# Optimization experiments

Measured on AMD Instinct MI355X. Metric: run time of the kernel, lower is better.

## Reference

```python
import jax, jax.numpy as jnp
import numpy as np

B, S, IN, H, C, L = 128, 512, 128, 512, 1000, 2


def setup_inputs() -> dict:
    key = jax.random.key(0)
    ks = jax.random.split(key, 11)
    s_in = 1.0 / np.sqrt(H)
    inp = {"x": jax.random.normal(ks[0], (B, S, IN), dtype=jnp.float32)}
    # layer 0
    inp["W_ih0"] = jax.random.uniform(ks[1], (H, IN), minval=-s_in, maxval=s_in)
    inp["W_hh0"] = jax.random.uniform(ks[2], (H, H), minval=-s_in, maxval=s_in)
    inp["b_ih0"] = jax.random.uniform(ks[3], (H,), minval=-s_in, maxval=s_in)
    inp["b_hh0"] = jax.random.uniform(ks[4], (H,), minval=-s_in, maxval=s_in)
    # layer 1
    inp["W_ih1"] = jax.random.uniform(ks[5], (H, H), minval=-s_in, maxval=s_in)
    inp["W_hh1"] = jax.random.uniform(ks[6], (H, H), minval=-s_in, maxval=s_in)
    inp["b_ih1"] = jax.random.uniform(ks[7], (H,), minval=-s_in, maxval=s_in)
    inp["b_hh1"] = jax.random.uniform(ks[8], (H,), minval=-s_in, maxval=s_in)
    # output linear
    inp["W_out"] = jax.random.uniform(ks[9], (C, H), minval=-s_in, maxval=s_in)
    inp["b_out"] = jax.random.uniform(ks[10], (C,), minval=-s_in, maxval=s_in)
    return inp


def _rnn_layer(seq, W_ih, W_hh, b_ih, b_hh):
    # seq: [B, S, D_in] -> [B, S, H]; h_t = tanh(x_t W_ih^T + b_ih + h_{t-1} W_hh^T + b_hh)
    # precompute input projection for all timesteps (one big GEMM)
    xp = jnp.einsum('bsd,hd->bsh', seq, W_ih) + b_ih + b_hh  # [B, S, H]
    h0 = jnp.zeros((seq.shape[0], W_hh.shape[0]), dtype=seq.dtype)

    def step(h, xp_t):
        h_new = jnp.tanh(xp_t + h @ W_hh.T)
        return h_new, h_new

    _, hs = jax.lax.scan(step, h0, jnp.swapaxes(xp, 0, 1))  # hs: [S, B, H]
    return jnp.swapaxes(hs, 0, 1)


def reference(x, W_ih0, W_hh0, b_ih0, b_hh0, W_ih1, W_hh1, b_ih1, b_hh1, W_out, b_out):
    h = _rnn_layer(x, W_ih0, W_hh0, b_ih0, b_hh0)
    h = _rnn_layer(h, W_ih1, W_hh1, b_ih1, b_hh1)
    logits = h[:, -1, :] @ W_out.T + b_out  # [B, C]
    return jax.nn.log_softmax(logits, axis=-1)
```

## Files before the change

### kernel.cpp

```cpp
#include <hip/hip_runtime.h>


using short8  = __attribute__((ext_vector_type(8))) short;
using floatx4 = __attribute__((ext_vector_type(4))) float;
using i32x4   = __attribute__((ext_vector_type(4))) int;
using f32x4   = __attribute__((ext_vector_type(4))) float;

#define DEV static __device__ __forceinline__
#define PINA(x) asm volatile("" : "+a"(x))
#define PINV(x) asm volatile("" : "+v"(x))

#define TWO_LOG2E 2.8853900817779268f

DEV void lds_barrier() {
    asm volatile("s_waitcnt lgkmcnt(0)\n\ts_barrier" ::: "memory");
}

DEV unsigned short f2bf(float f) {
    union { float f; unsigned u; } v; v.f = f;
    unsigned r = (v.u + 0x7fffu + ((v.u >> 16) & 1u)) >> 16;
    return (unsigned short)r;
}

__global__ __launch_bounds__(64) void packi8_kernel(
    const float* __restrict__ W, signed char* __restrict__ Wq,
    float* __restrict__ sc2)
{
    const int j = blockIdx.x;
    const int t = threadIdx.x;
    const float* row = W + (size_t)j * 512;

    float4 a = *(const float4*)(row + t * 8);
    float4 b = *(const float4*)(row + t * 8 + 4);
    float m = fmaxf(fmaxf(fabsf(a.x), fabsf(a.y)), fmaxf(fabsf(a.z), fabsf(a.w)));
    m = fmaxf(m, fmaxf(fmaxf(fabsf(b.x), fabsf(b.y)), fmaxf(fabsf(b.z), fabsf(b.w))));
    #pragma unroll
    for (int off = 32; off; off >>= 1) m = fmaxf(m, __shfl_down(m, off, 64));
    m = __shfl(m, 0, 64);
    if (t == 0) sc2[j] = m * (1.0f / (127.f * 127.f)) * TWO_LOG2E;

    if (t < 32) {
        const int kt = t >> 2, lq = t & 3;
        const int jtg = j >> 4, lm = j & 15;
        const float r = 127.f / m;
        int w4[4];
        #pragma unroll
        for (int w = 0; w < 4; ++w) {
            int v = 0;
            #pragma unroll
            for (int e = 0; e < 4; ++e) {
                int q = __float2int_rn(row[kt * 64 + lq * 16 + w * 4 + e] * r);
                v |= (q & 255) << (8 * e);
            }
            w4[w] = v;
        }
        i32x4 pk; pk[0] = w4[0]; pk[1] = w4[1]; pk[2] = w4[2]; pk[3] = w4[3];
        *(i32x4*)(Wq + ((size_t)((jtg * 8 + kt) * 64 + lq * 16 + lm)) * 16) = pk;
    }
}

template <int K, int MODE>
__global__ __launch_bounds__(256, 2) void proj_kernel(
    const void* __restrict__ Aptr, const float* __restrict__ W,
    const float* __restrict__ b1, const float* __restrict__ b2,
    unsigned short* __restrict__ out, float oscale)
{
    constexpr int LDA = 40;
    __shared__ unsigned short As[128 * LDA];
    __shared__ unsigned short Ws[64 * LDA];

    const int tid  = threadIdx.x;
    const int lane = tid & 63, wave = tid >> 6;
    const int lm   = lane & 15, lq = lane >> 4;
    const int nbase = blockIdx.x * 64;
    const int mtile = blockIdx.y;
    const int mbase = mtile * 128;

    floatx4 acc[2][4] = {};

    const int ar = tid >> 1, ak = (tid & 1) * 16;
    const int wr = tid >> 2, wk = (tid & 3) * 8;

    for (int k0 = 0; k0 < K; k0 += 32) {
        if (MODE == 0) {
            const float* x   = (const float*)Aptr;
            const float* src = x + ((size_t)ar * 512 + mtile) * 128 + (k0 + ak);
            float4 f0 = *(const float4*)(src + 0);
            float4 f1 = *(const float4*)(src + 4);
            float4 f2 = *(const float4*)(src + 8);
            float4 f3 = *(const float4*)(src + 12);
            unsigned short* d = As + ar * LDA + ak;
            d[0]=f2bf(f0.x); d[1]=f2bf(f0.y); d[2]=f2bf(f0.z); d[3]=f2bf(f0.w);
            d[4]=f2bf(f1.x); d[5]=f2bf(f1.y); d[6]=f2bf(f1.z); d[7]=f2bf(f1.w);
            d[8]=f2bf(f2.x); d[9]=f2bf(f2.y); d[10]=f2bf(f2.z); d[11]=f2bf(f2.w);
            d[12]=f2bf(f3.x); d[13]=f2bf(f3.y); d[14]=f2bf(f3.z); d[15]=f2bf(f3.w);
        } else {
            const unsigned short* h =
                (const unsigned short*)Aptr + (size_t)(mbase + ar) * K + k0 + ak;
            short8 v0 = *(const short8*)(h);
            short8 v1 = *(const short8*)(h + 8);
            *(short8*)(As + ar * LDA + ak)     = v0;
            *(short8*)(As + ar * LDA + ak + 8) = v1;
        }
        {
            const float* src = W + (size_t)(nbase + wr) * K + k0 + wk;
            float4 f0 = *(const float4*)(src);
            float4 f1 = *(const float4*)(src + 4);
            unsigned short* d = Ws + wr * LDA + wk;
            d[0]=f2bf(f0.x); d[1]=f2bf(f0.y); d[2]=f2bf(f0.z); d[3]=f2bf(f0.w);
            d[4]=f2bf(f1.x); d[5]=f2bf(f1.y); d[6]=f2bf(f1.z); d[7]=f2bf(f1.w);
        }
        __syncthreads();

        short8 af0 = *(const short8*)(As + (wave * 32 +  0 + lm) * LDA + lq * 8);
        short8 af1 = *(const short8*)(As + (wave * 32 + 16 + lm) * LDA + lq * 8);
        #pragma unroll
        for (int nt = 0; nt < 4; ++nt) {
            short8 bf = *(const short8*)(Ws + (nt * 16 + lm) * LDA + lq * 8);
            acc[0][nt] = __builtin_amdgcn_mfma_f32_16x16x32_bf16(af0, bf, acc[0][nt], 0, 0, 0);
            acc[1][nt] = __builtin_amdgcn_mfma_f32_16x16x32_bf16(af1, bf, acc[1][nt], 0, 0, 0);
        }
        __syncthreads();
    }

    #pragma unroll
    for (int nt = 0; nt < 4; ++nt) {
        const int n = nbase + nt * 16 + lm;
        const float bias = b1[n] + b2[n];
        #pragma unroll
        for (int mt = 0; mt < 2; ++mt) {
            const int mrow = mbase + wave * 32 + mt * 16 + lq * 4;
            #pragma unroll
            for (int r = 0; r < 4; ++r)
                out[(size_t)(mrow + r) * 512 + n] = f2bf((acc[mt][nt][r] + bias) * oscale);
        }
    }
}


#define MFMA_J(JJ, BFR)                                                        \
  {                                                                            \
    acc[JJ] = __builtin_amdgcn_mfma_i32_16x16x64_i8(wa[JJ][0], BFR[0], z4, 0, 0, 0); \
    _Pragma("unroll")                                                          \
    for (int kt = 1; kt < 8; ++kt)                                             \
      acc[JJ] = __builtin_amdgcn_mfma_i32_16x16x64_i8(wa[JJ][kt], BFR[kt], acc[JJ], 0, 0, 0); \
  }

#define EPI_J(JJ, XVROW, HWBUF, TCUR)                                          \
  {                                                                            \
    const int jtg = wave * 4 + (JJ);                                           \
    float x0 = __uint_as_float(__builtin_amdgcn_perm(XVROW[JJ].x, 0u, 0x05040c0cu)); \
    float x1 = __uint_as_float(__builtin_amdgcn_perm(XVROW[JJ].x, 0u, 0x07060c0cu)); \
    float x2 = __uint_as_float(__builtin_amdgcn_perm(XVROW[JJ].y, 0u, 0x05040c0cu)); \
    float x3 = __uint_as_float(__builtin_amdgcn_perm(XVROW[JJ].y, 0u, 0x07060c0cu)); \
    float e0 = __builtin_amdgcn_exp2f(fmaf((float)acc[JJ][0], sc[JJ][0], x0));  \
    float e1 = __builtin_amdgcn_exp2f(fmaf((float)acc[JJ][1], sc[JJ][1], x1));  \
    float e2 = __builtin_amdgcn_exp2f(fmaf((float)acc[JJ][2], sc[JJ][2], x2));  \
    float e3 = __builtin_amdgcn_exp2f(fmaf((float)acc[JJ][3], sc[JJ][3], x3));  \
    float q0 = fmaf(-2.f, __builtin_amdgcn_rcpf(e0 + 1.f), 1.f);                \
    float q1 = fmaf(-2.f, __builtin_amdgcn_rcpf(e1 + 1.f), 1.f);                \
    float q2 = fmaf(-2.f, __builtin_amdgcn_rcpf(e2 + 1.f), 1.f);                \
    float q3 = fmaf(-2.f, __builtin_amdgcn_rcpf(e3 + 1.f), 1.f);                \
    unsigned m0 = __float_as_uint(fmaf(q0, 127.f, 12582912.f));                 \
    unsigned m1 = __float_as_uint(fmaf(q1, 127.f, 12582912.f));                 \
    unsigned m2 = __float_as_uint(fmaf(q2, 127.f, 12582912.f));                 \
    unsigned m3 = __float_as_uint(fmaf(q3, 127.f, 12582912.f));                 \
    unsigned lo = __builtin_amdgcn_perm(m1, m0, 0x00000400u);                   \
    unsigned hi = __builtin_amdgcn_perm(m3, m2, 0x00000400u);                   \
    unsigned qb = __builtin_amdgcn_perm(hi, lo, 0x05040100u);                   \
    *(unsigned*)((HWBUF) + lm * 512 + ((jtg ^ lm) << 4) + lq * 4) = qb;         \
    if (MODE == 0) {                                                            \
      if (lm < 2) {                                                             \
        uint2 st;                                                               \
        st.x = __builtin_amdgcn_perm(__float_as_uint(q1), __float_as_uint(q0), 0x07060302u); \
        st.y = __builtin_amdgcn_perm(__float_as_uint(q3), __float_as_uint(q2), 0x07060302u); \
        *(uint2*)(hst + (JJ) * 16) = st;                                        \
      }                                                                         \
    } else if ((TCUR) == 511) {                                                 \
      if (lm < 2) {                                                             \
        float4 o; o.x = q0; o.y = q1; o.z = q2; o.w = q3;                       \
        *(float4*)(h_last + (size_t)bb * 512 + jtg * 16 + lq * 4) = o;          \
      }                                                                         \
    }                                                                           \
  }

#define REC_STEP(P, TCUR)                                                      \
  {                                                                            \
    i32x4 bfr[8];                                                              \
    _Pragma("unroll")                                                          \
    for (int kt = 0; kt < 8; ++kt)                                             \
      bfr[kt] = *(const i32x4*)(&h2[P][0] + lm * 512 + ((((kt << 2) + lq)) ^ lm) * 16); \
    if ((TCUR) < 511) {                                                        \
      _Pragma("unroll")                                                        \
      for (int j = 0; j < 4; ++j)                                              \
        xv[(P) ^ 1][j] = *(const uint2*)(xpt + j * 16);                        \
      xpt += 65536;                                                            \
    }                                                                          \
    MFMA_J(0, bfr);                                                            \
    _Pragma("unroll")                                                          \
    for (int j = 1; j < 4; ++j) {                                              \
      MFMA_J(j, bfr);                                                          \
      EPI_J(j - 1, xv[P], &h2[(P) ^ 1][0], TCUR);                              \
    }                                                                          \
    EPI_J(3, xv[P], &h2[(P) ^ 1][0], TCUR);                                    \
    if (MODE == 0) hst += 65536;                                               \
    lds_barrier();                                                             \
  }

template <int MODE>
__global__ __launch_bounds__(512, 2) void rec12_kernel(
    const signed char* __restrict__ Wq,
    const float* __restrict__ sc2,
    const unsigned short* xp,
    unsigned short* hs_out,
    float* __restrict__ h_last)
{
    __shared__ unsigned char h2[2][16 * 512];

    const int tid  = threadIdx.x;
    const int lane = tid & 63;
    const int wave = tid >> 6;
    const int lm   = lane & 15, lq = lane >> 4;
    const int bg   = blockIdx.x;
    const int bb   = bg * 2 + (lm & 1);

    i32x4 wa[4][8];
    #pragma unroll
    for (int j = 0; j < 4; ++j) {
        const int jtg = wave * 4 + j;
        #pragma unroll
        for (int kt = 0; kt < 8; ++kt)
            wa[j][kt] = *(const i32x4*)(Wq + ((size_t)((jtg * 8 + kt) * 64 + lane)) * 16);
    }
    #pragma unroll
    for (int j = 0; j < 4; ++j)
        #pragma unroll
        for (int kt = 0; kt < 8; ++kt)
            PINA(wa[j][kt]);

    f32x4 sc[4];
    #pragma unroll
    for (int j = 0; j < 4; ++j)
        sc[j] = *(const f32x4*)(sc2 + (wave * 4 + j) * 16 + lq * 4);
    #pragma unroll
    for (int j = 0; j < 4; ++j) PINV(sc[j]);

    for (int i = tid; i < 4096; i += 512) ((int*)h2)[i] = 0;
    __syncthreads();

    const unsigned short* xpt = xp + (size_t)bb * 512 + wave * 64 + lq * 4;
    unsigned short*       hst = hs_out + (size_t)bb * 512 + wave * 64 + lq * 4;

    uint2 xv[2][4];
    i32x4 acc[4];
    const i32x4 z4 = {0, 0, 0, 0};

    #pragma unroll
    for (int j = 0; j < 4; ++j) xv[0][j] = *(const uint2*)(xpt + j * 16);
    xpt += 65536;

    for (int t = 0; t < 512; t += 2) {
        REC_STEP(0, t);
        REC_STEP(1, t + 1);
    }
}

__global__ __launch_bounds__(256, 2) void head_kernel(
    const float* __restrict__ hl, const float* __restrict__ Wout,
    const float* __restrict__ bout, float* __restrict__ out)
{
    __shared__ float hrow[512];
    __shared__ float lg[1000];
    __shared__ float red[8];
    const int b = blockIdx.x, tid = threadIdx.x;

    hrow[tid]       = hl[(size_t)b * 512 + tid];
    hrow[tid + 256] = hl[(size_t)b * 512 + 256 + tid];
    __syncthreads();

    float lmax = -1e30f;
    for (int c = tid; c < 1000; c += 256) {
        const float4* w4 = (const float4*)(Wout + (size_t)c * 512);
        float a0 = 0.f, a1 = 0.f, a2 = 0.f, a3 = 0.f;
        #pragma unroll 4
        for (int k = 0; k < 128; ++k) {
            float4 w = w4[k];
            a0 += hrow[4 * k + 0] * w.x;
            a1 += hrow[4 * k + 1] * w.y;
            a2 += hrow[4 * k + 2] * w.z;
            a3 += hrow[4 * k + 3] * w.w;
        }
        float acc = bout[c] + (a0 + a1) + (a2 + a3);
        lg[c] = acc;
        lmax = fmaxf(lmax, acc);
    }
    #pragma unroll
    for (int off = 32; off; off >>= 1) lmax = fmaxf(lmax, __shfl_down(lmax, off, 64));
    if ((tid & 63) == 0) red[tid >> 6] = lmax;
    __syncthreads();
    if (tid == 0) red[4] = fmaxf(fmaxf(red[0], red[1]), fmaxf(red[2], red[3]));
    __syncthreads();
    const float M = red[4];

    float lsum = 0.f;
    for (int c = tid; c < 1000; c += 256) lsum += __expf(lg[c] - M);
    #pragma unroll
    for (int off = 32; off; off >>= 1) lsum += __shfl_down(lsum, off, 64);
    __syncthreads();
    if ((tid & 63) == 0) red[tid >> 6] = lsum;
    __syncthreads();
    if (tid == 0) red[5] = M + __logf(red[0] + red[1] + red[2] + red[3]);
    __syncthreads();
    const float lse = red[5];

    for (int c = tid; c < 1000; c += 256)
        out[(size_t)b * 1000 + c] = lg[c] - lse;
}

extern "C" void kernel_launch(void* const* d_in, const int* in_sizes, int n_in,
                              void* d_out, int out_size, void* d_ws, size_t ws_size,
                              hipStream_t stream)
{
    const float* x    = (const float*)d_in[0];
    const float* Wih0 = (const float*)d_in[1];
    const float* Whh0 = (const float*)d_in[2];
    const float* bih0 = (const float*)d_in[3];
    const float* bhh0 = (const float*)d_in[4];
    const float* Wih1 = (const float*)d_in[5];
    const float* Whh1 = (const float*)d_in[6];
    const float* bih1 = (const float*)d_in[7];
    const float* bhh1 = (const float*)d_in[8];
    const float* Wout = (const float*)d_in[9];
    const float* bout = (const float*)d_in[10];
    float* out = (float*)d_out;

    char* ws = (char*)d_ws;
    unsigned short* bufA = (unsigned short*)ws;
    unsigned short* bufB = (unsigned short*)(ws + (size_t)64 * 1024 * 1024);
    signed char* Wq0 = (signed char*)bufB;
    float*       sc0 = (float*)((char*)bufB + 262144);
    signed char* Wq1 = (signed char*)bufA;
    float*       sc1 = (float*)(ws + 262144);
    float*     hlast = (float*)(ws + (size_t)1 * 1024 * 1024);

    const dim3 pgrid(8, 512);

    packi8_kernel<<<512, 64, 0, stream>>>(Whh0, Wq0, sc0);
    proj_kernel<128, 0><<<pgrid, 256, 0, stream>>>((const void*)x, Wih0, bih0, bhh0, bufA, TWO_LOG2E);
    rec12_kernel<0><<<64, 512, 0, stream>>>(Wq0, sc0, bufA, bufA, hlast);

    proj_kernel<512, 1><<<pgrid, 256, 0, stream>>>((const void*)bufA, Wih1, bih1, bhh1, bufB, TWO_LOG2E);
    packi8_kernel<<<512, 64, 0, stream>>>(Whh1, Wq1, sc1);
    rec12_kernel<1><<<64, 512, 0, stream>>>(Wq1, sc1, bufB, bufB, hlast);

    head_kernel<<<128, 256, 0, stream>>>(hlast, Wout, bout, out);
}
```

Baseline: 1.658 ms.

## Spread recurrence over one batch row per block; use fp16 projections with fma_mix

Result: faster. 1.512 ms (-8.8%).

```diff
diff --git a/kernel.cpp b/kernel.cpp
--- a/kernel.cpp
+++ b/kernel.cpp
@@ -20,6 +20,11 @@
     union { float f; unsigned u; } v; v.f = f;
     unsigned r = (v.u + 0x7fffu + ((v.u >> 16) & 1u)) >> 16;
     return (unsigned short)r;
+}
+
+DEV unsigned short f2h(float f) {
+    union { _Float16 h; unsigned short u; } c; c.h = (_Float16)f;
+    return c.u;
 }
 
 __global__ __launch_bounds__(64) void packi8_kernel(
@@ -132,7 +137,7 @@
             const int mrow = mbase + wave * 32 + mt * 16 + lq * 4;
             #pragma unroll
             for (int r = 0; r < 4; ++r)
-                out[(size_t)(mrow + r) * 512 + n] = f2bf((acc[mt][nt][r] + bias) * oscale);
+                out[(size_t)(mrow + r) * 512 + n] = f2h((acc[mt][nt][r] + bias) * oscale);
         }
     }
 }
@@ -149,14 +154,21 @@
 #define EPI_J(JJ, XVROW, HWBUF, TCUR)                                          \
   {                                                                            \
     const int jtg = wave * 4 + (JJ);                                           \
-    float x0 = __uint_as_float(__builtin_amdgcn_perm(XVROW[JJ].x, 0u, 0x05040c0cu)); \
-    float x1 = __uint_as_float(__builtin_amdgcn_perm(XVROW[JJ].x, 0u, 0x07060c0cu)); \
-    float x2 = __uint_as_float(__builtin_amdgcn_perm(XVROW[JJ].y, 0u, 0x05040c0cu)); \
-    float x3 = __uint_as_float(__builtin_amdgcn_perm(XVROW[JJ].y, 0u, 0x07060c0cu)); \
-    float e0 = __builtin_amdgcn_exp2f(fmaf((float)acc[JJ][0], sc[JJ][0], x0));  \
-    float e1 = __builtin_amdgcn_exp2f(fmaf((float)acc[JJ][1], sc[JJ][1], x1));  \
-    float e2 = __builtin_amdgcn_exp2f(fmaf((float)acc[JJ][2], sc[JJ][2], x2));  \
-    float e3 = __builtin_amdgcn_exp2f(fmaf((float)acc[JJ][3], sc[JJ][3], x3));  \
+    float a0 = (float)acc[JJ][0], a1 = (float)acc[JJ][1];                       \
+    float a2 = (float)acc[JJ][2], a3 = (float)acc[JJ][3];                       \
+    float z0, z1, z2, z3;                                                       \
+    asm("v_fma_mix_f32 %0, %1, %2, %3 op_sel:[0,0,0] op_sel_hi:[0,0,1]"         \
+        : "=v"(z0) : "v"(a0), "v"(sc[JJ][0]), "v"(XVROW[JJ].x));                \
+    asm("v_fma_mix_f32 %0, %1, %2, %3 op_sel:[0,0,1] op_sel_hi:[0,0,1]"         \
+        : "=v"(z1) : "v"(a1), "v"(sc[JJ][1]), "v"(XVROW[JJ].x));                \
+    asm("v_fma_mix_f32 %0, %1, %2, %3 op_sel:[0,0,0] op_sel_hi:[0,0,1]"         \
+        : "=v"(z2) : "v"(a2), "v"(sc[JJ][2]), "v"(XVROW[JJ].y));                \
+    asm("v_fma_mix_f32 %0, %1, %2, %3 op_sel:[0,0,1] op_sel_hi:[0,0,1]"         \
+        : "=v"(z3) : "v"(a3), "v"(sc[JJ][3]), "v"(XVROW[JJ].y));                \
+    float e0 = __builtin_amdgcn_exp2f(z0);                                      \
+    float e1 = __builtin_amdgcn_exp2f(z1);                                      \
+    float e2 = __builtin_amdgcn_exp2f(z2);                                      \
+    float e3 = __builtin_amdgcn_exp2f(z3);                                      \
     float q0 = fmaf(-2.f, __builtin_amdgcn_rcpf(e0 + 1.f), 1.f);                \
     float q1 = fmaf(-2.f, __builtin_amdgcn_rcpf(e1 + 1.f), 1.f);                \
     float q2 = fmaf(-2.f, __builtin_amdgcn_rcpf(e2 + 1.f), 1.f);                \
@@ -170,14 +182,14 @@
     unsigned qb = __builtin_amdgcn_perm(hi, lo, 0x05040100u);                   \
     *(unsigned*)((HWBUF) + lm * 512 + ((jtg ^ lm) << 4) + lq * 4) = qb;         \
     if (MODE == 0) {                                                            \
-      if (lm < 2) {                                                             \
+      if (st_en) {                                                              \
         uint2 st;                                                               \
         st.x = __builtin_amdgcn_perm(__float_as_uint(q1), __float_as_uint(q0), 0x07060302u); \
         st.y = __builtin_amdgcn_perm(__float_as_uint(q3), __float_as_uint(q2), 0x07060302u); \
         *(uint2*)(hst + (JJ) * 16) = st;                                        \
       }                                                                         \
     } else if ((TCUR) == 511) {                                                 \
-      if (lm < 2) {                                                             \
+      if (st_en) {                                                              \
         float4 o; o.x = q0; o.y = q1; o.z = q2; o.w = q3;                       \
         *(float4*)(h_last + (size_t)bb * 512 + jtg * 16 + lq * 4) = o;          \
       }                                                                         \
@@ -208,7 +220,7 @@
   }
 
 template <int MODE>
-__global__ __launch_bounds__(512, 2) void rec12_kernel(
+__global__ __launch_bounds__(512, 2) void rec13_kernel(
     const signed char* __restrict__ Wq,
     const float* __restrict__ sc2,
     const unsigned short* xp,
@@ -222,7 +234,8 @@
     const int wave = tid >> 6;
     const int lm   = lane & 15, lq = lane >> 4;
     const int bg   = blockIdx.x;
-    const int bb   = bg * 2 + (lm & 1);
+    const int bb   = bg >> 1;
+    const bool st_en = ((bg & 1) == 0) && (lm == 0);
 
     i32x4 wa[4][8];
     #pragma unroll
@@ -347,11 +360,11 @@
 
     packi8_kernel<<<512, 64, 0, stream>>>(Whh0, Wq0, sc0);
     proj_kernel<128, 0><<<pgrid, 256, 0, stream>>>((const void*)x, Wih0, bih0, bhh0, bufA, TWO_LOG2E);
-    rec12_kernel<0><<<64, 512, 0, stream>>>(Wq0, sc0, bufA, bufA, hlast);
+    rec13_kernel<0><<<256, 512, 0, stream>>>(Wq0, sc0, bufA, bufA, hlast);
 
     proj_kernel<512, 1><<<pgrid, 256, 0, stream>>>((const void*)bufA, Wih1, bih1, bhh1, bufB, TWO_LOG2E);
     packi8_kernel<<<512, 64, 0, stream>>>(Whh1, Wq1, sc1);
-    rec12_kernel<1><<<64, 512, 0, stream>>>(Wq1, sc1, bufB, bufB, hlast);
+    rec13_kernel<1><<<256, 512, 0, stream>>>(Wq1, sc1, bufB, bufB, hlast);
 
     head_kernel<<<128, 256, 0, stream>>>(hlast, Wout, bout, out);
 }
```
